# Kernel optimization log

Hardware: AMD Instinct MI355X
Metric: run time of the kernel (lower is better)

## Reference

```python
import jax, jax.numpy as jnp
import numpy as np

BLOCK = 128          # block_size in the source
FP8_MAX = 448.0      # max representable magnitude of float8_e4m3fn


def _quant_weight(w):
    """Pre-quantize a [N, K] float weight into fp8 values + per 128x128 block scales."""
    N, K = w.shape
    wb = w.reshape(N // BLOCK, BLOCK, K // BLOCK, BLOCK)
    w_scale = jnp.max(jnp.abs(wb), axis=(1, 3)) / FP8_MAX           # [Nb, Kb]
    s = jnp.where(w_scale == 0, 1.0, w_scale)
    wq = (wb / s[:, None, :, None]).astype(jnp.float8_e4m3fn).astype(jnp.float32)
    return wq.reshape(N, K), w_scale


def setup_inputs() -> dict:
    key = jax.random.key(0)
    kx, kw = jax.random.split(key)
    M, K, N = 16384, 2048, 2048
    x = jax.random.normal(kx, (M, K), dtype=jnp.float32)
    w = jax.random.normal(kw, (N, K), dtype=jnp.float32) * 0.02
    w_fp8, w_scale = _quant_weight(w)
    return {"x": x, "w_fp8": w_fp8, "w_scale": w_scale}


def reference(x, w_fp8, w_scale):
    """fp8 block-quantized linear: act_quant(x) then dequantized GEMM.

    x:       [M, K] float32 activations
    w_fp8:   [N, K] fp8-valued weight (stored as float32, exactly e4m3 representable)
    w_scale: [N/128, K/128] per-block weight scales
    """
    M, K = x.shape
    N = w_fp8.shape[0]
    # --- act_quant: per 128-element block along K, scale = amax / 448 ---
    xb = x.reshape(M, K // BLOCK, BLOCK)
    x_scale = jnp.max(jnp.abs(xb), axis=-1) / FP8_MAX               # [M, Kb]
    sx = jnp.where(x_scale == 0, 1.0, x_scale)
    xq = (xb / sx[..., None]).astype(jnp.float8_e4m3fn).astype(jnp.float32)
    # --- fp8_gemm with inline dequant: scales factor out per (m-block, n-block, k-block)
    # sum_kb sx[m,kb]*sw[nb,kb]*(xq . wq) == (xq*sx) @ (wq*sw)^T exactly ---
    x_deq = (xq * sx[..., None]).reshape(M, K)
    w_deq = (w_fp8.reshape(N // BLOCK, BLOCK, K // BLOCK, BLOCK)
             * w_scale[:, None, :, None]).reshape(N, K)
    return x_deq @ w_deq.T                                          # [M, N]
```

## Files before the change

kernel.cpp:

```cpp
#include <hip/hip_runtime.h>

#define M_DIM 16384
#define N_DIM 2048
#define K_DIM 2048
#define KB    (K_DIM / 128)

#define BM 256
#define BN 256
#define BK 64
#define NT (K_DIM / BK)

#define XGRID (M_DIM * K_DIM / 1024)
#define WGRID (N_DIM * K_DIM / 1024)

typedef __bf16 bf16x8 __attribute__((ext_vector_type(8)));
typedef float  f32x4  __attribute__((ext_vector_type(4)));

__device__ __forceinline__ unsigned short f32_to_bf16_rne(float f) {
    unsigned int u = __float_as_uint(f);
    u += 0x7FFFu + ((u >> 16) & 1u);
    return (unsigned short)(u >> 16);
}

__global__ __launch_bounds__(256) void quant_all_kernel(const float* __restrict__ x,
                                                        unsigned short* __restrict__ xdq,
                                                        const float* __restrict__ w,
                                                        const float* __restrict__ wscale,
                                                        unsigned short* __restrict__ wdq) {
    const int tid = threadIdx.x;
    if (blockIdx.x < XGRID) {
        const size_t base = ((size_t)blockIdx.x * 256 + tid) * 4;
        const float4 v = *(const float4*)(x + base);
        float amax = fmaxf(fmaxf(fabsf(v.x), fabsf(v.y)), fmaxf(fabsf(v.z), fabsf(v.w)));
#pragma unroll
        for (int m = 16; m >= 1; m >>= 1)
            amax = fmaxf(amax, __shfl_xor(amax, m, 64));
        float s = amax / 448.0f;
        if (s == 0.0f) s = 1.0f;
        const int p01 = __builtin_amdgcn_cvt_pk_fp8_f32(v.x / s, v.y / s, 0, false);
        const int p23 = __builtin_amdgcn_cvt_pk_fp8_f32(v.z / s, v.w / s, 0, false);
        const float d0 = __builtin_amdgcn_cvt_f32_fp8(p01, 0) * s;
        const float d1 = __builtin_amdgcn_cvt_f32_fp8(p01, 1) * s;
        const float d2 = __builtin_amdgcn_cvt_f32_fp8(p23, 0) * s;
        const float d3 = __builtin_amdgcn_cvt_f32_fp8(p23, 1) * s;
        uint2 out;
        out.x = (unsigned int)f32_to_bf16_rne(d0) | ((unsigned int)f32_to_bf16_rne(d1) << 16);
        out.y = (unsigned int)f32_to_bf16_rne(d2) | ((unsigned int)f32_to_bf16_rne(d3) << 16);
        *(uint2*)(xdq + base) = out;
    } else {
        const size_t e = ((size_t)(blockIdx.x - XGRID) * 256 + tid) * 4;
        const float4 v = *(const float4*)(w + e);
        const int n = (int)(e >> 11);
        const int k = (int)(e & 2047);
        const float s = wscale[(n >> 7) * KB + (k >> 7)];
        uint2 out;
        out.x = (unsigned int)f32_to_bf16_rne(v.x * s) | ((unsigned int)f32_to_bf16_rne(v.y * s) << 16);
        out.y = (unsigned int)f32_to_bf16_rne(v.z * s) | ((unsigned int)f32_to_bf16_rne(v.w * s) << 16);
        *(uint2*)(wdq + e) = out;
    }
}

__global__ __launch_bounds__(512, 2) void gemm_bt_kernel(const unsigned short* __restrict__ A,
                                                         const unsigned short* __restrict__ B,
                                                         float* __restrict__ C) {
    __shared__ __align__(16) unsigned short As[2][BM * BK];
    __shared__ __align__(16) unsigned short Bs[2][BN * BK];

    const int tid  = threadIdx.x;
    const int lane = tid & 63;
    const int wave = tid >> 6;
    const int wm   = (wave >> 2) * 128;
    const int wn   = (wave & 3) * 64;
    const int quad = lane >> 4;
    const int l16  = lane & 15;

    const int m0 = blockIdx.x * BM;
    const int n0 = blockIdx.y * BN;

    f32x4 acc[8][4] = {};

    const int srow = tid >> 3;
    const int scol = (tid & 7) ^ (srow & 7);
    const unsigned short* gA = A + (size_t)(m0 + srow) * K_DIM + scol * 8;
    const unsigned short* gB = B + (size_t)(n0 + srow) * K_DIM + scol * 8;

#define STAGE_A(NXT, i, ktn) \
    __builtin_amdgcn_global_load_lds( \
        (__attribute__((address_space(1))) void*)(gA + (size_t)((i) * 64) * K_DIM + (ktn) * BK), \
        (__attribute__((address_space(3))) void*)(&As[NXT][(i) * 4096 + wave * 512]), 16, 0, 0)
#define STAGE_B(NXT, i, ktn) \
    __builtin_amdgcn_global_load_lds( \
        (__attribute__((address_space(1))) void*)(gB + (size_t)((i) * 64) * K_DIM + (ktn) * BK), \
        (__attribute__((address_space(3))) void*)(&Bs[NXT][(i) * 4096 + wave * 512]), 16, 0, 0)

#define VMCNT(n) asm volatile("s_waitcnt vmcnt(" #n ")" ::: "memory")

#define PHASE(CUR, MI0, NJ0, WAIT, ...) do { \
    bf16x8 af[4][2], bfr[2][2]; \
    _Pragma("unroll") \
    for (int i = 0; i < 4; ++i) { \
      _Pragma("unroll") \
      for (int kk = 0; kk < 2; ++kk) \
        af[i][kk] = *(const bf16x8*)(&As[CUR][(wm + ((MI0) + i) * 16 + l16) * BK + ((kk * 4 + quad) ^ (l16 & 7)) * 8]); \
    } \
    _Pragma("unroll") \
    for (int j = 0; j < 2; ++j) { \
      _Pragma("unroll") \
      for (int kk = 0; kk < 2; ++kk) \
        bfr[j][kk] = *(const bf16x8*)(&Bs[CUR][(wn + ((NJ0) + j) * 16 + l16) * BK + ((kk * 4 + quad) ^ (l16 & 7)) * 8]); \
    } \
    __VA_ARGS__; \
    __builtin_amdgcn_s_barrier(); \
    asm volatile("s_waitcnt lgkmcnt(0)" ::: "memory"); \
    __builtin_amdgcn_s_setprio(1); \
    _Pragma("unroll") \
    for (int i = 0; i < 4; ++i) { \
      _Pragma("unroll") \
      for (int j = 0; j < 2; ++j) { \
        acc[(MI0) + i][(NJ0) + j] = __builtin_amdgcn_mfma_f32_16x16x32_bf16(af[i][0], bfr[j][0], acc[(MI0) + i][(NJ0) + j], 0, 0, 0); \
        acc[(MI0) + i][(NJ0) + j] = __builtin_amdgcn_mfma_f32_16x16x32_bf16(af[i][1], bfr[j][1], acc[(MI0) + i][(NJ0) + j], 0, 0, 0); \
      } \
    } \
    __builtin_amdgcn_s_setprio(0); \
    WAIT; \
    __builtin_amdgcn_s_barrier(); \
  } while (0)

#define TILE_FULL(CUR, NXT, KTN) do { \
    PHASE(CUR, 0, 0, (void)0, STAGE_B(NXT, 0, KTN); STAGE_B(NXT, 1, KTN); STAGE_B(NXT, 2, KTN)); \
    PHASE(CUR, 0, 2, VMCNT(6), STAGE_B(NXT, 3, KTN); STAGE_A(NXT, 0, KTN); STAGE_A(NXT, 2, KTN)); \
    PHASE(CUR, 4, 0, (void)0, STAGE_A(NXT, 1, KTN); STAGE_A(NXT, 3, KTN)); \
    PHASE(CUR, 4, 2, VMCNT(2), (void)0); \
  } while (0)

#define TILE_LAST(CUR) do { \
    PHASE(CUR, 0, 0, (void)0, (void)0); \
    PHASE(CUR, 0, 2, VMCNT(0), (void)0); \
    PHASE(CUR, 4, 0, (void)0, (void)0); \
    PHASE(CUR, 4, 2, (void)0, (void)0); \
  } while (0)

    STAGE_B(0, 0, 0); STAGE_B(0, 1, 0); STAGE_B(0, 2, 0); STAGE_B(0, 3, 0);
    STAGE_A(0, 0, 0); STAGE_A(0, 2, 0); STAGE_A(0, 1, 0); STAGE_A(0, 3, 0);
    VMCNT(2);
    __builtin_amdgcn_s_barrier();

    for (int kt = 0; kt < NT - 2; kt += 2) {
        TILE_FULL(0, 1, kt + 1);
        TILE_FULL(1, 0, kt + 2);
    }
    TILE_FULL(0, 1, NT - 1);
    TILE_LAST(1);

#pragma unroll
    for (int i = 0; i < 8; ++i) {
        const int row = m0 + wm + i * 16 + quad * 4;
#pragma unroll
        for (int j = 0; j < 4; ++j) {
            const int col = n0 + wn + j * 16 + l16;
            float* cp = C + (size_t)row * N_DIM + col;
#pragma unroll
            for (int r = 0; r < 4; ++r)
                cp[(size_t)r * N_DIM] = acc[i][j][r];
        }
    }
}

extern "C" void kernel_launch(void* const* d_in, const int* in_sizes, int n_in,
                              void* d_out, int out_size, void* d_ws, size_t ws_size,
                              hipStream_t stream) {
    const float* x      = (const float*)d_in[0];
    const float* wfp8   = (const float*)d_in[1];
    const float* wscale = (const float*)d_in[2];
    float* out = (float*)d_out;

    unsigned short* xdq = (unsigned short*)d_ws;
    unsigned short* wdq = xdq + (size_t)M_DIM * K_DIM;

    quant_all_kernel<<<XGRID + WGRID, 256, 0, stream>>>(x, xdq, wfp8, wscale, wdq);
    gemm_bt_kernel<<<dim3(M_DIM / BM, N_DIM / BN), 512, 0, stream>>>(xdq, wdq, out);
}
```

Baseline: 380.7 us.

## Split LDS tiles into K-halves with deeper staged pipeline; widen quant kernel

The GEMM shared-memory layout changes to [buf][k-half][256][32] with a new XOR swizzle. The main loop now runs four phases per pair of tiles, each computing one 32-wide K half over the full 8x4 accumulator grid. Loads are issued one half-tile further ahead, with a vmcnt wait and a single barrier per phase, which removes the mid-phase barrier and lgkmcnt wait. Separately, the quant kernel processes 8 elements per thread with 16-byte stores and half as many blocks. The costs are more live fragment registers per phase and a new swizzle whose bank-conflict behaviour is not yet checked.

```diff
diff --git a/kernel.cpp b/kernel.cpp
--- a/kernel.cpp
+++ b/kernel.cpp
@@ -10,8 +10,8 @@
 #define BK 64
 #define NT (K_DIM / BK)
 
-#define XGRID (M_DIM * K_DIM / 1024)
-#define WGRID (N_DIM * K_DIM / 1024)
+#define XGRID (M_DIM * K_DIM / 2048)
+#define WGRID (N_DIM * K_DIM / 2048)
 
 typedef __bf16 bf16x8 __attribute__((ext_vector_type(8)));
 typedef float  f32x4  __attribute__((ext_vector_type(4)));
@@ -29,42 +29,52 @@
                                                         unsigned short* __restrict__ wdq) {
     const int tid = threadIdx.x;
     if (blockIdx.x < XGRID) {
-        const size_t base = ((size_t)blockIdx.x * 256 + tid) * 4;
-        const float4 v = *(const float4*)(x + base);
-        float amax = fmaxf(fmaxf(fabsf(v.x), fabsf(v.y)), fmaxf(fabsf(v.z), fabsf(v.w)));
+        const size_t base = ((size_t)blockIdx.x * 256 + tid) * 8;
+        const float4 va = *(const float4*)(x + base);
+        const float4 vb = *(const float4*)(x + base + 4);
+        float amax = fmaxf(
+            fmaxf(fmaxf(fabsf(va.x), fabsf(va.y)), fmaxf(fabsf(va.z), fabsf(va.w))),
+            fmaxf(fmaxf(fabsf(vb.x), fabsf(vb.y)), fmaxf(fabsf(vb.z), fabsf(vb.w))));
 #pragma unroll
-        for (int m = 16; m >= 1; m >>= 1)
+        for (int m = 8; m >= 1; m >>= 1)
             amax = fmaxf(amax, __shfl_xor(amax, m, 64));
         float s = amax / 448.0f;
         if (s == 0.0f) s = 1.0f;
-        const int p01 = __builtin_amdgcn_cvt_pk_fp8_f32(v.x / s, v.y / s, 0, false);
-        const int p23 = __builtin_amdgcn_cvt_pk_fp8_f32(v.z / s, v.w / s, 0, false);
-        const float d0 = __builtin_amdgcn_cvt_f32_fp8(p01, 0) * s;
-        const float d1 = __builtin_amdgcn_cvt_f32_fp8(p01, 1) * s;
-        const float d2 = __builtin_amdgcn_cvt_f32_fp8(p23, 0) * s;
-        const float d3 = __builtin_amdgcn_cvt_f32_fp8(p23, 1) * s;
-        uint2 out;
-        out.x = (unsigned int)f32_to_bf16_rne(d0) | ((unsigned int)f32_to_bf16_rne(d1) << 16);
-        out.y = (unsigned int)f32_to_bf16_rne(d2) | ((unsigned int)f32_to_bf16_rne(d3) << 16);
-        *(uint2*)(xdq + base) = out;
+        const int p01 = __builtin_amdgcn_cvt_pk_fp8_f32(va.x / s, va.y / s, 0, false);
+        const int p23 = __builtin_amdgcn_cvt_pk_fp8_f32(va.z / s, va.w / s, 0, false);
+        const int p45 = __builtin_amdgcn_cvt_pk_fp8_f32(vb.x / s, vb.y / s, 0, false);
+        const int p67 = __builtin_amdgcn_cvt_pk_fp8_f32(vb.z / s, vb.w / s, 0, false);
+        uint4 out;
+        out.x = (unsigned int)f32_to_bf16_rne(__builtin_amdgcn_cvt_f32_fp8(p01, 0) * s)
+              | ((unsigned int)f32_to_bf16_rne(__builtin_amdgcn_cvt_f32_fp8(p01, 1) * s) << 16);
+        out.y = (unsigned int)f32_to_bf16_rne(__builtin_amdgcn_cvt_f32_fp8(p23, 0) * s)
+              | ((unsigned int)f32_to_bf16_rne(__builtin_amdgcn_cvt_f32_fp8(p23, 1) * s) << 16);
+        out.z = (unsigned int)f32_to_bf16_rne(__builtin_amdgcn_cvt_f32_fp8(p45, 0) * s)
+              | ((unsigned int)f32_to_bf16_rne(__builtin_amdgcn_cvt_f32_fp8(p45, 1) * s) << 16);
+        out.w = (unsigned int)f32_to_bf16_rne(__builtin_amdgcn_cvt_f32_fp8(p67, 0) * s)
+              | ((unsigned int)f32_to_bf16_rne(__builtin_amdgcn_cvt_f32_fp8(p67, 1) * s) << 16);
+        *(uint4*)(xdq + base) = out;
     } else {
-        const size_t e = ((size_t)(blockIdx.x - XGRID) * 256 + tid) * 4;
-        const float4 v = *(const float4*)(w + e);
+        const size_t e = ((size_t)(blockIdx.x - XGRID) * 256 + tid) * 8;
+        const float4 va = *(const float4*)(w + e);
+        const float4 vb = *(const float4*)(w + e + 4);
         const int n = (int)(e >> 11);
         const int k = (int)(e & 2047);
         const float s = wscale[(n >> 7) * KB + (k >> 7)];
-        uint2 out;
-        out.x = (unsigned int)f32_to_bf16_rne(v.x * s) | ((unsigned int)f32_to_bf16_rne(v.y * s) << 16);
-        out.y = (unsigned int)f32_to_bf16_rne(v.z * s) | ((unsigned int)f32_to_bf16_rne(v.w * s) << 16);
-        *(uint2*)(wdq + e) = out;
+        uint4 out;
+        out.x = (unsigned int)f32_to_bf16_rne(va.x * s) | ((unsigned int)f32_to_bf16_rne(va.y * s) << 16);
+        out.y = (unsigned int)f32_to_bf16_rne(va.z * s) | ((unsigned int)f32_to_bf16_rne(va.w * s) << 16);
+        out.z = (unsigned int)f32_to_bf16_rne(vb.x * s) | ((unsigned int)f32_to_bf16_rne(vb.y * s) << 16);
+        out.w = (unsigned int)f32_to_bf16_rne(vb.z * s) | ((unsigned int)f32_to_bf16_rne(vb.w * s) << 16);
+        *(uint4*)(wdq + e) = out;
     }
 }
 
 __global__ __launch_bounds__(512, 2) void gemm_bt_kernel(const unsigned short* __restrict__ A,
                                                          const unsigned short* __restrict__ B,
                                                          float* __restrict__ C) {
-    __shared__ __align__(16) unsigned short As[2][BM * BK];
-    __shared__ __align__(16) unsigned short Bs[2][BN * BK];
+    __shared__ __align__(16) unsigned short As[2][2][256][32];
+    __shared__ __align__(16) unsigned short Bs[2][2][256][32];
 
     const int tid  = threadIdx.x;
     const int lane = tid & 63;
@@ -73,84 +83,70 @@
     const int wn   = (wave & 3) * 64;
     const int quad = lane >> 4;
     const int l16  = lane & 15;
+    const int pc   = quad ^ ((l16 >> 1) & 3);
 
     const int m0 = blockIdx.x * BM;
     const int n0 = blockIdx.y * BN;
 
     f32x4 acc[8][4] = {};
 
-    const int srow = tid >> 3;
-    const int scol = (tid & 7) ^ (srow & 7);
-    const unsigned short* gA = A + (size_t)(m0 + srow) * K_DIM + scol * 8;
-    const unsigned short* gB = B + (size_t)(n0 + srow) * K_DIM + scol * 8;
+    const int srow = tid >> 2;
+    const int sc   = (tid & 3) ^ ((tid >> 3) & 3);
+    const unsigned short* gA = A + (size_t)(m0 + srow) * K_DIM + sc * 8;
+    const unsigned short* gB = B + (size_t)(n0 + srow) * K_DIM + sc * 8;
 
-#define STAGE_A(NXT, i, ktn) \
-    __builtin_amdgcn_global_load_lds( \
-        (__attribute__((address_space(1))) void*)(gA + (size_t)((i) * 64) * K_DIM + (ktn) * BK), \
-        (__attribute__((address_space(3))) void*)(&As[NXT][(i) * 4096 + wave * 512]), 16, 0, 0)
-#define STAGE_B(NXT, i, ktn) \
-    __builtin_amdgcn_global_load_lds( \
-        (__attribute__((address_space(1))) void*)(gB + (size_t)((i) * 64) * K_DIM + (ktn) * BK), \
-        (__attribute__((address_space(3))) void*)(&Bs[NXT][(i) * 4096 + wave * 512]), 16, 0, 0)
+#define GLD(SRC, DST) __builtin_amdgcn_global_load_lds( \
+    (__attribute__((address_space(1))) void*)(SRC), \
+    (__attribute__((address_space(3))) void*)(DST), 16, 0, 0)
+
+#define STAGE4(BUF, KH, KT) do { \
+    GLD(gA + (size_t)(KT) * 64 + (KH) * 32,                       &As[BUF][KH][wave * 16][0]); \
+    GLD(gA + (size_t)128 * K_DIM + (size_t)(KT) * 64 + (KH) * 32, &As[BUF][KH][128 + wave * 16][0]); \
+    GLD(gB + (size_t)(KT) * 64 + (KH) * 32,                       &Bs[BUF][KH][wave * 16][0]); \
+    GLD(gB + (size_t)128 * K_DIM + (size_t)(KT) * 64 + (KH) * 32, &Bs[BUF][KH][128 + wave * 16][0]); \
+  } while (0)
 
 #define VMCNT(n) asm volatile("s_waitcnt vmcnt(" #n ")" ::: "memory")
+#define BAR() __builtin_amdgcn_s_barrier()
 
-#define PHASE(CUR, MI0, NJ0, WAIT, ...) do { \
-    bf16x8 af[4][2], bfr[2][2]; \
+#define PHASE(BUF, KK, WAIT, STAGES) do { \
+    STAGES; \
+    bf16x8 af[8], bfr[4]; \
     _Pragma("unroll") \
-    for (int i = 0; i < 4; ++i) { \
-      _Pragma("unroll") \
-      for (int kk = 0; kk < 2; ++kk) \
-        af[i][kk] = *(const bf16x8*)(&As[CUR][(wm + ((MI0) + i) * 16 + l16) * BK + ((kk * 4 + quad) ^ (l16 & 7)) * 8]); \
-    } \
+    for (int i = 0; i < 8; ++i) \
+      af[i] = *(const bf16x8*)(&As[BUF][KK][wm + i * 16 + l16][pc * 8]); \
     _Pragma("unroll") \
-    for (int j = 0; j < 2; ++j) { \
-      _Pragma("unroll") \
-      for (int kk = 0; kk < 2; ++kk) \
-        bfr[j][kk] = *(const bf16x8*)(&Bs[CUR][(wn + ((NJ0) + j) * 16 + l16) * BK + ((kk * 4 + quad) ^ (l16 & 7)) * 8]); \
-    } \
-    __VA_ARGS__; \
-    __builtin_amdgcn_s_barrier(); \
-    asm volatile("s_waitcnt lgkmcnt(0)" ::: "memory"); \
+    for (int j = 0; j < 4; ++j) \
+      bfr[j] = *(const bf16x8*)(&Bs[BUF][KK][wn + j * 16 + l16][pc * 8]); \
     __builtin_amdgcn_s_setprio(1); \
     _Pragma("unroll") \
-    for (int i = 0; i < 4; ++i) { \
+    for (int i = 0; i < 8; ++i) { \
       _Pragma("unroll") \
-      for (int j = 0; j < 2; ++j) { \
-        acc[(MI0) + i][(NJ0) + j] = __builtin_amdgcn_mfma_f32_16x16x32_bf16(af[i][0], bfr[j][0], acc[(MI0) + i][(NJ0) + j], 0, 0, 0); \
-        acc[(MI0) + i][(NJ0) + j] = __builtin_amdgcn_mfma_f32_16x16x32_bf16(af[i][1], bfr[j][1], acc[(MI0) + i][(NJ0) + j], 0, 0, 0); \
-      } \
+      for (int j = 0; j < 4; ++j) \
+        acc[i][j] = __builtin_amdgcn_mfma_f32_16x16x32_bf16(af[i], bfr[j], acc[i][j], 0, 0, 0); \
     } \
     __builtin_amdgcn_s_setprio(0); \
     WAIT; \
-    __builtin_amdgcn_s_barrier(); \
+    BAR(); \
   } while (0)
 
-#define TILE_FULL(CUR, NXT, KTN) do { \
-    PHASE(CUR, 0, 0, (void)0, STAGE_B(NXT, 0, KTN); STAGE_B(NXT, 1, KTN); STAGE_B(NXT, 2, KTN)); \
-    PHASE(CUR, 0, 2, VMCNT(6), STAGE_B(NXT, 3, KTN); STAGE_A(NXT, 0, KTN); STAGE_A(NXT, 2, KTN)); \
-    PHASE(CUR, 4, 0, (void)0, STAGE_A(NXT, 1, KTN); STAGE_A(NXT, 3, KTN)); \
-    PHASE(CUR, 4, 2, VMCNT(2), (void)0); \
-  } while (0)
+    STAGE4(0, 0, 0);
+    STAGE4(0, 1, 0);
+    STAGE4(1, 0, 1);
+    VMCNT(8);
+    BAR();
 
-#define TILE_LAST(CUR) do { \
-    PHASE(CUR, 0, 0, (void)0, (void)0); \
-    PHASE(CUR, 0, 2, VMCNT(0), (void)0); \
-    PHASE(CUR, 4, 0, (void)0, (void)0); \
-    PHASE(CUR, 4, 2, (void)0, (void)0); \
-  } while (0)
-
-    STAGE_B(0, 0, 0); STAGE_B(0, 1, 0); STAGE_B(0, 2, 0); STAGE_B(0, 3, 0);
-    STAGE_A(0, 0, 0); STAGE_A(0, 2, 0); STAGE_A(0, 1, 0); STAGE_A(0, 3, 0);
-    VMCNT(2);
-    __builtin_amdgcn_s_barrier();
-
-    for (int kt = 0; kt < NT - 2; kt += 2) {
-        TILE_FULL(0, 1, kt + 1);
-        TILE_FULL(1, 0, kt + 2);
+#pragma unroll 1
+    for (int t = 0; t < NT - 2; t += 2) {
+        PHASE(0, 0, VMCNT(8), STAGE4(1, 1, t + 1));
+        PHASE(0, 1, VMCNT(8), STAGE4(0, 0, t + 2));
+        PHASE(1, 0, VMCNT(8), STAGE4(0, 1, t + 2));
+        PHASE(1, 1, VMCNT(8), STAGE4(1, 0, t + 3));
     }
-    TILE_FULL(0, 1, NT - 1);
-    TILE_LAST(1);
+    PHASE(0, 0, VMCNT(8), STAGE4(1, 1, NT - 1));
+    PHASE(0, 1, VMCNT(4), (void)0);
+    PHASE(1, 0, VMCNT(0), (void)0);
+    PHASE(1, 1, (void)0, (void)0);
 
 #pragma unroll
     for (int i = 0; i < 8; ++i) {
```

Measured after the change: 371.1 us. 2.5% less time.
